# Performance work log

Hardware: AMD Instinct MI355X
Metric: run time of the kernel (lower is better)

The kernel has to match this reference:

```python
import jax, jax.numpy as jnp
import numpy as np

BN_EPS = 1e-5


def setup_inputs() -> dict:
    key = jax.random.key(0)
    ks = jax.random.split(key, 10)
    B, C, L = 16, 512, 1024
    scale = 1.0 / np.sqrt(C)
    inp = {
        "x": jax.random.normal(ks[0], (B, C, L), dtype=jnp.float32),
        "gamma": jnp.ones((C,), jnp.float32),
        "beta": jnp.zeros((C,), jnp.float32),
        "Wq": jax.random.normal(ks[1], (C, C), jnp.float32) * scale,
        "bq": jnp.zeros((C,), jnp.float32),
        "Wk": jax.random.normal(ks[2], (C, C), jnp.float32) * scale,
        "bk": jnp.zeros((C,), jnp.float32),
        "Wv": jax.random.normal(ks[3], (C, C), jnp.float32) * scale,
        "bv": jnp.zeros((C,), jnp.float32),
        "Wp": jax.random.normal(ks[4], (C, C), jnp.float32) * scale,
        "bp": jnp.zeros((C,), jnp.float32),
    }
    return inp


def _pointwise(W, b, h):
    # Conv1d with kernel_size=1 == per-position linear: [C_out,C_in] x [B,C_in,L]
    return jnp.einsum("oc,bcl->bol", W, h) + b[None, :, None]


def reference(x, gamma, beta, Wq, bq, Wk, bk, Wv, bv, Wp, bp):
    B, C, L = x.shape
    # BatchNorm1d (training-mode batch statistics over batch & length dims)
    mean = jnp.mean(x, axis=(0, 2), keepdims=True)
    var = jnp.var(x, axis=(0, 2), keepdims=True)
    hn = (x - mean) * jax.lax.rsqrt(var + BN_EPS)
    hn = hn * gamma[None, :, None] + beta[None, :, None]

    q = _pointwise(Wq, bq, hn)  # [B,C,L]
    k = _pointwise(Wk, bk, hn)
    v = _pointwise(Wv, bv, hn)

    # attn[b,i,j] = sum_c q[b,c,i] k[b,c,j] / sqrt(C); i=query pos, j=key pos
    attn = jnp.einsum("bci,bcj->bij", q, k) * (C ** -0.5)
    attn = jax.nn.softmax(attn, axis=-1)

    # out[b,c,i] = sum_j attn[b,i,j] v[b,c,j]
    h_ = jnp.einsum("bij,bcj->bci", attn, v)
    h_ = _pointwise(Wp, bp, h_)
    return x + h_
```

## Files before the change

### kernel.cpp

```cpp
#include <hip/hip_runtime.h>
#include <hip/hip_bf16.h>


#define BB 16
#define CC 512
#define LL 1024

typedef __bf16 bf16x8 __attribute__((ext_vector_type(8)));
typedef float  f32x4  __attribute__((ext_vector_type(4)));

__device__ inline unsigned short bf16_bits(float f) {
  __hip_bfloat16 h = __float2bfloat16(f);
  return __builtin_bit_cast(unsigned short, h);
}
__device__ inline float bits_lo(unsigned int u) {
  return __builtin_bit_cast(float, u << 16);
}
__device__ inline float bits_hi(unsigned int u) {
  return __builtin_bit_cast(float, u & 0xffff0000u);
}

__global__ __launch_bounds__(256) void bn_stats(
    const float* __restrict__ x, const float* __restrict__ gamma,
    const float* __restrict__ beta, float* __restrict__ scl,
    float* __restrict__ sft) {
  int c = blockIdx.x;
  int t = threadIdx.x;
  float s = 0.f, s2 = 0.f;
  for (int b = 0; b < BB; ++b) {
    float4 v = ((const float4*)(x + ((size_t)(b * CC + c)) * LL))[t];
    s  += v.x + v.y + v.z + v.w;
    s2 += v.x * v.x + v.y * v.y + v.z * v.z + v.w * v.w;
  }
  for (int m = 32; m; m >>= 1) { s += __shfl_xor(s, m, 64); s2 += __shfl_xor(s2, m, 64); }
  __shared__ float rs[4], rs2[4];
  int wave = t >> 6, lane = t & 63;
  if (lane == 0) { rs[wave] = s; rs2[wave] = s2; }
  __syncthreads();
  if (t == 0) {
    float S  = rs[0] + rs[1] + rs[2] + rs[3];
    float S2 = rs2[0] + rs2[1] + rs2[2] + rs2[3];
    float mean = S * (1.f / 16384.f);
    float var  = S2 * (1.f / 16384.f) - mean * mean;
    float sc = gamma[c] * rsqrtf(var + 1e-5f);
    scl[c] = sc;
    sft[c] = beta[c] - mean * sc;
  }
}

__global__ __launch_bounds__(256) void cast4(
    const float* __restrict__ Wq, const float* __restrict__ Wk,
    const float* __restrict__ Wv, const float* __restrict__ Wp,
    __hip_bfloat16* __restrict__ Wqkv, __hip_bfloat16* __restrict__ Wpb) {
  int m = blockIdx.y;
  const float* src = m == 0 ? Wq : m == 1 ? Wk : m == 2 ? Wv : Wp;
  __hip_bfloat16* dst = m < 3 ? Wqkv + (size_t)m * 262144 : Wpb;
  int i = blockIdx.x * 256 + threadIdx.x;
  float4 v = ((const float4*)src)[i];
  ushort4 o;
  o.x = bf16_bits(v.x); o.y = bf16_bits(v.y);
  o.z = bf16_bits(v.z); o.w = bf16_bits(v.w);
  ((ushort4*)dst)[i] = o;
}

__global__ __launch_bounds__(256) void norm_t(
    const float* __restrict__ x, const float* __restrict__ scl,
    const float* __restrict__ sft, __hip_bfloat16* __restrict__ hnT) {
  __shared__ float tile[32][33];
  int l0 = blockIdx.x * 32, c0 = blockIdx.y * 32, b = blockIdx.z;
  int t = threadIdx.x;
#pragma unroll
  for (int i = 0; i < 4; ++i) {
    int idx = t + i * 256;
    int cc = idx >> 5, ll = idx & 31;
    tile[cc][ll] = x[((size_t)(b * CC + c0 + cc)) * LL + l0 + ll];
  }
  __syncthreads();
#pragma unroll
  for (int i = 0; i < 2; ++i) {
    int idx = t + i * 256;
    int ll = idx >> 4, cc = (idx & 15) * 2;
    float v0 = tile[cc][ll] * scl[c0 + cc] + sft[c0 + cc];
    float v1 = tile[cc + 1][ll] * scl[c0 + cc + 1] + sft[c0 + cc + 1];
    ushort2 o; o.x = bf16_bits(v0); o.y = bf16_bits(v1);
    *(ushort2*)(hnT + ((size_t)(b * LL + l0 + ll)) * CC + c0 + cc) = o;
  }
}

__global__ __launch_bounds__(256) void softmax_bf16(__hip_bfloat16* __restrict__ S) {
  int wave = threadIdx.x >> 6, lane = threadIdx.x & 63;
  size_t row = (size_t)blockIdx.x * 4 + wave;
  uint4* p = (uint4*)(S + row * 1024);
  uint4 r0 = p[lane * 2], r1 = p[lane * 2 + 1];
  float f[16];
  unsigned int w[8] = {r0.x, r0.y, r0.z, r0.w, r1.x, r1.y, r1.z, r1.w};
#pragma unroll
  for (int i = 0; i < 8; ++i) { f[2 * i] = bits_lo(w[i]); f[2 * i + 1] = bits_hi(w[i]); }
  float mx = f[0];
#pragma unroll
  for (int i = 1; i < 16; ++i) mx = fmaxf(mx, f[i]);
  for (int m = 32; m; m >>= 1) mx = fmaxf(mx, __shfl_xor(mx, m, 64));
  float s = 0.f;
#pragma unroll
  for (int i = 0; i < 16; ++i) { f[i] = __expf(f[i] - mx); s += f[i]; }
  for (int m = 32; m; m >>= 1) s += __shfl_xor(s, m, 64);
  float inv = 1.f / s;
  unsigned int ow[8];
#pragma unroll
  for (int i = 0; i < 8; ++i) {
    unsigned int lo = bf16_bits(f[2 * i] * inv);
    unsigned int hi = bf16_bits(f[2 * i + 1] * inv);
    ow[i] = lo | (hi << 16);
  }
  uint4 o0 = {ow[0], ow[1], ow[2], ow[3]}, o1 = {ow[4], ow[5], ow[6], ow[7]};
  p[lane * 2] = o0; p[lane * 2 + 1] = o1;
}

__device__ __forceinline__ void gemm_core(
    const __hip_bfloat16* __restrict__ A, int lda,
    const __hip_bfloat16* __restrict__ B, int ldb, int K,
    __hip_bfloat16* sA, __hip_bfloat16* sB, f32x4 (&acc)[4][4]) {
  const int tid = threadIdx.x;
  const int wave = tid >> 6, lane = tid & 63;
  const int wm = (wave >> 1) * 64, wn = (wave & 1) * 64;
  const int row0 = tid >> 2;
  const int ke0 = (((tid & 3) ^ ((tid >> 3) & 3)) * 8);
  const int fr = lane & 15;
  const int q = lane >> 4;
  const int colA = ((q ^ ((fr >> 1) & 3)) * 8);
  for (int k0 = 0; k0 < K; k0 += 32) {
    __syncthreads();
#pragma unroll
    for (int it = 0; it < 2; ++it) {
      const __hip_bfloat16* ga = A + (size_t)(it * 64 + row0) * lda + (k0 + ke0);
      const __hip_bfloat16* gb = B + (size_t)(it * 64 + row0) * ldb + (k0 + ke0);
      __builtin_amdgcn_global_load_lds(
          (__attribute__((address_space(1))) void*)(void*)ga,
          (__attribute__((address_space(3))) void*)(sA + (it * 256 + wave * 64) * 8),
          16, 0, 0);
      __builtin_amdgcn_global_load_lds(
          (__attribute__((address_space(1))) void*)(void*)gb,
          (__attribute__((address_space(3))) void*)(sB + (it * 256 + wave * 64) * 8),
          16, 0, 0);
    }
    __syncthreads();
    bf16x8 af[4], bfr[4];
#pragma unroll
    for (int i = 0; i < 4; ++i) {
      af[i]  = *(const bf16x8*)(sA + (wm + i * 16 + fr) * 32 + colA);
      bfr[i] = *(const bf16x8*)(sB + (wn + i * 16 + fr) * 32 + colA);
    }
#pragma unroll
    for (int i = 0; i < 4; ++i)
#pragma unroll
      for (int j = 0; j < 4; ++j)
        acc[i][j] = __builtin_amdgcn_mfma_f32_16x16x32_bf16(af[i], bfr[j], acc[i][j], 0, 0, 0);
  }
}

__global__ __launch_bounds__(256, 3) void gemm_qkv(
    const __hip_bfloat16* __restrict__ Wb, const __hip_bfloat16* __restrict__ hnT,
    __hip_bfloat16* __restrict__ qT, __hip_bfloat16* __restrict__ kT,
    __hip_bfloat16* __restrict__ vN,
    const float* __restrict__ bq, const float* __restrict__ bk,
    const float* __restrict__ bv) {
  __shared__ __align__(16) __hip_bfloat16 sA[128 * 32];
  __shared__ __align__(16) __hip_bfloat16 sB[128 * 32];
  const int bat = blockIdx.z;
  const int m0 = blockIdx.y * 128, n0 = blockIdx.x * 128;
  f32x4 acc[4][4] = {};
  gemm_core(Wb + (size_t)m0 * 512, 512,
            hnT + (size_t)bat * LL * CC + (size_t)n0 * 512, 512, 512, sA, sB, acc);
  const int lane = threadIdx.x & 63, wave = threadIdx.x >> 6;
  const int wm = (wave >> 1) * 64, wn = (wave & 1) * 64;
  const int crow = (lane >> 4) * 4, ccol = lane & 15;
  const int id = m0 >> 9;
  const int mloc0 = m0 & 511;
  const float* bias = id == 0 ? bq : id == 1 ? bk : bv;
  if (id < 2) {
    __hip_bfloat16* D = (id == 0 ? qT : kT) + (size_t)bat * LL * CC;
#pragma unroll
    for (int i = 0; i < 4; ++i) {
      int mg = mloc0 + wm + i * 16 + crow;
      float bv4[4];
#pragma unroll
      for (int r = 0; r < 4; ++r) bv4[r] = bias[mg + r];
#pragma unroll
      for (int j = 0; j < 4; ++j) {
        int ng = n0 + wn + j * 16 + ccol;
        ushort4 o;
        o.x = bf16_bits(acc[i][j][0] + bv4[0]);
        o.y = bf16_bits(acc[i][j][1] + bv4[1]);
        o.z = bf16_bits(acc[i][j][2] + bv4[2]);
        o.w = bf16_bits(acc[i][j][3] + bv4[3]);
        *(ushort4*)(D + (size_t)ng * 512 + mg) = o;
      }
    }
  } else {
    __hip_bfloat16* D = vN + (size_t)bat * CC * LL;
#pragma unroll
    for (int i = 0; i < 4; ++i) {
      int mg = mloc0 + wm + i * 16 + crow;
      float bv4[4];
#pragma unroll
      for (int r = 0; r < 4; ++r) bv4[r] = bias[mg + r];
#pragma unroll
      for (int j = 0; j < 4; ++j) {
        int ng = n0 + wn + j * 16 + ccol;
#pragma unroll
        for (int r = 0; r < 4; ++r)
          D[(size_t)(mg + r) * 1024 + ng] = __float2bfloat16(acc[i][j][r] + bv4[r]);
      }
    }
  }
}

template <int MODE, bool BIAS>
__global__ __launch_bounds__(256, 3) void gemm_tn(
    const __hip_bfloat16* __restrict__ A, int lda, size_t strideA,
    const __hip_bfloat16* __restrict__ B, int ldb, size_t strideB,
    void* __restrict__ Dp, int ldd, size_t strideD,
    const float* __restrict__ bias, float scale,
    const float* __restrict__ resid, size_t strideR, int K) {
  __shared__ __align__(16) __hip_bfloat16 sA[128 * 32];
  __shared__ __align__(16) __hip_bfloat16 sB[128 * 32];
  const int bat = blockIdx.z;
  const int m0 = blockIdx.y * 128, n0 = blockIdx.x * 128;
  f32x4 acc[4][4] = {};
  gemm_core(A + (size_t)bat * strideA + (size_t)m0 * lda, lda,
            B + (size_t)bat * strideB + (size_t)n0 * ldb, ldb, K, sA, sB, acc);
  const int lane = threadIdx.x & 63, wave = threadIdx.x >> 6;
  const int wm = (wave >> 1) * 64, wn = (wave & 1) * 64;
  const int crow = (lane >> 4) * 4, ccol = lane & 15;
  if constexpr (MODE == 0) {
    __hip_bfloat16* D = (__hip_bfloat16*)Dp + (size_t)bat * strideD;
#pragma unroll
    for (int i = 0; i < 4; ++i) {
      int mg = m0 + wm + i * 16 + crow;
      float bv4[4];
#pragma unroll
      for (int r = 0; r < 4; ++r) bv4[r] = BIAS ? bias[mg + r] : 0.f;
#pragma unroll
      for (int j = 0; j < 4; ++j) {
        int ng = n0 + wn + j * 16 + ccol;
#pragma unroll
        for (int r = 0; r < 4; ++r)
          D[(size_t)(mg + r) * ldd + ng] =
              __float2bfloat16(acc[i][j][r] * scale + bv4[r]);
      }
    }
  } else {
    float* D = (float*)Dp + (size_t)bat * strideD;
#pragma unroll
    for (int i = 0; i < 4; ++i) {
      int mg = m0 + wm + i * 16 + crow;
      float bv4[4];
#pragma unroll
      for (int r = 0; r < 4; ++r) bv4[r] = BIAS ? bias[mg + r] : 0.f;
#pragma unroll
      for (int j = 0; j < 4; ++j) {
        int ng = n0 + wn + j * 16 + ccol;
        const float* rsrc = resid + (size_t)bat * strideR + (size_t)mg * ldd + ng;
        float* dst = D + (size_t)mg * ldd + ng;
#pragma unroll
        for (int r = 0; r < 4; ++r)
          dst[(size_t)r * ldd] = acc[i][j][r] * scale + bv4[r] + rsrc[(size_t)r * ldd];
      }
    }
  }
}

extern "C" void kernel_launch(void* const* d_in, const int* in_sizes, int n_in,
                              void* d_out, int out_size, void* d_ws, size_t ws_size,
                              hipStream_t stream) {
  const float* x     = (const float*)d_in[0];
  const float* gamma = (const float*)d_in[1];
  const float* beta  = (const float*)d_in[2];
  const float* Wq    = (const float*)d_in[3];
  const float* bq    = (const float*)d_in[4];
  const float* Wk    = (const float*)d_in[5];
  const float* bk    = (const float*)d_in[6];
  const float* Wv    = (const float*)d_in[7];
  const float* bv    = (const float*)d_in[8];
  const float* Wp    = (const float*)d_in[9];
  const float* bp    = (const float*)d_in[10];
  float* out = (float*)d_out;

  char* ws = (char*)d_ws;
  float* scl = (float*)ws;
  float* sft = scl + 512;
  __hip_bfloat16* Wqkvb = (__hip_bfloat16*)(ws + 4096);
  __hip_bfloat16* Wpb = Wqkvb + 786432;
  __hip_bfloat16* hnT = Wpb + 262144;
  __hip_bfloat16* qT  = hnT + 8388608;
  __hip_bfloat16* kT  = qT + 8388608;
  __hip_bfloat16* vN  = kT + 8388608;
  __hip_bfloat16* Sb  = vN + 8388608;
  __hip_bfloat16* HT  = hnT;

  bn_stats<<<512, 256, 0, stream>>>(x, gamma, beta, scl, sft);
  cast4<<<dim3(256, 4), 256, 0, stream>>>(Wq, Wk, Wv, Wp, Wqkvb, Wpb);
  norm_t<<<dim3(32, 16, 16), 256, 0, stream>>>(x, scl, sft, hnT);

  const size_t sLC = (size_t)LL * CC;
  const size_t sCL = (size_t)CC * LL;
  const size_t sLLb = (size_t)LL * LL;

  gemm_qkv<<<dim3(8, 12, 16), 256, 0, stream>>>(Wqkvb, hnT, qT, kT, vN, bq, bk, bv);
  gemm_tn<0, false><<<dim3(8, 8, 16), 256, 0, stream>>>(
      qT, 512, sLC, kT, 512, sLC, Sb, 1024, sLLb, nullptr,
      0.04419417382415922f, nullptr, 0, 512);
  softmax_bf16<<<4096, 256, 0, stream>>>(Sb);
  gemm_tn<0, false><<<dim3(4, 8, 16), 256, 0, stream>>>(
      Sb, 1024, sLLb, vN, 1024, sCL, HT, 512, sLC, nullptr, 1.f, nullptr, 0, 1024);
  gemm_tn<3, true><<<dim3(8, 4, 16), 256, 0, stream>>>(
      Wpb, 512, 0, HT, 512, sLC, out, 1024, sCL, bp, 1.f, x, sCL, 512);
}
```

Baseline: 244.2 us.

## Use 256x256-tile triple-buffered GEMM core for QKV and score GEMMs

Adds a 512-thread GEMM core with 256x256 output tiles, three-stage LDS buffering via direct global-to-LDS loads, and explicit waitcnt/barrier scheduling with raised priority around the MFMA block. The QKV projection is relaunched as one flattened GEMM over batch times length, and QK^T uses the new core. The aim is more data reuse per tile and overlap of loads with compute, so the GEMMs spend less time waiting on memory. In exchange it uses more registers and LDS and launches fewer blocks, which may reduce occupancy and leave some CUs idle.

After: 249.5 us. 1.02x slower.

```diff
diff --git a/kernel.cpp b/kernel.cpp
--- a/kernel.cpp
+++ b/kernel.cpp
@@ -158,59 +158,171 @@
   }
 }
 
-__global__ __launch_bounds__(256, 3) void gemm_qkv(
+__device__ __forceinline__ void gemm_core256(
+    const __hip_bfloat16* __restrict__ A, int lda,
+    const __hip_bfloat16* __restrict__ B, int ldb, int K,
+    __hip_bfloat16* sA, __hip_bfloat16* sB, f32x4 (&acc)[8][4]) {
+  const int tid = threadIdx.x;
+  const int wave = tid >> 6, lane = tid & 63;
+  const int row0 = tid >> 2;
+  const int ke0 = (((tid & 3) ^ ((tid >> 3) & 3)) * 8);
+  const int fr = lane & 15;
+  const int q = lane >> 4;
+  const int colA = ((q ^ ((fr >> 1) & 3)) * 8);
+  const int wm = (wave >> 2) * 128, wn = (wave & 3) * 64;
+  const int NT = K >> 5;
+
+  const __hip_bfloat16* ga0 = A + (size_t)row0 * lda + ke0;
+  const __hip_bfloat16* gb0 = B + (size_t)row0 * ldb + ke0;
+  __hip_bfloat16* dA = sA + wave * 512;
+  __hip_bfloat16* dB = sB + wave * 512;
+
+#define STAGE256(tt, ss)                                                       \
+  {                                                                            \
+    const __hip_bfloat16* ga = ga0 + (tt) * 32;                                \
+    const __hip_bfloat16* gb = gb0 + (tt) * 32;                                \
+    __builtin_amdgcn_global_load_lds(                                          \
+        (__attribute__((address_space(1))) void*)(void*)ga,                    \
+        (__attribute__((address_space(3))) void*)(dA + (ss) * 8192), 16, 0, 0);\
+    __builtin_amdgcn_global_load_lds(                                          \
+        (__attribute__((address_space(1))) void*)(void*)(ga + (size_t)128 * lda), \
+        (__attribute__((address_space(3))) void*)(dA + (ss) * 8192 + 4096), 16, 0, 0); \
+    __builtin_amdgcn_global_load_lds(                                          \
+        (__attribute__((address_space(1))) void*)(void*)gb,                    \
+        (__attribute__((address_space(3))) void*)(dB + (ss) * 8192), 16, 0, 0);\
+    __builtin_amdgcn_global_load_lds(                                          \
+        (__attribute__((address_space(1))) void*)(void*)(gb + (size_t)128 * ldb), \
+        (__attribute__((address_space(3))) void*)(dB + (ss) * 8192 + 4096), 16, 0, 0); \
+  }
+
+  STAGE256(0, 0);
+  if (NT > 1) STAGE256(1, 1);
+  if (NT > 2) STAGE256(2, 2);
+
+  int s = 0;
+  for (int t = 0; t < NT; ++t) {
+    if (t < NT - 2) {
+      asm volatile("s_waitcnt vmcnt(8)" ::: "memory");
+    } else if (t == NT - 2) {
+      asm volatile("s_waitcnt vmcnt(4)" ::: "memory");
+    } else {
+      asm volatile("s_waitcnt vmcnt(0)" ::: "memory");
+    }
+    __builtin_amdgcn_s_barrier();
+    __builtin_amdgcn_sched_barrier(0);
+
+    const __hip_bfloat16* pA = sA + s * 8192;
+    const __hip_bfloat16* pB = sB + s * 8192;
+    bf16x8 af[8], bfr[4];
+#pragma unroll
+    for (int i = 0; i < 8; ++i)
+      af[i] = *(const bf16x8*)(pA + (wm + i * 16 + fr) * 32 + colA);
+#pragma unroll
+    for (int j = 0; j < 4; ++j)
+      bfr[j] = *(const bf16x8*)(pB + (wn + j * 16 + fr) * 32 + colA);
+    asm volatile("s_waitcnt lgkmcnt(0)" ::: "memory");
+    __builtin_amdgcn_sched_barrier(0);
+    __builtin_amdgcn_s_barrier();
+    __builtin_amdgcn_sched_barrier(0);
+
+    if (t + 3 < NT) STAGE256(t + 3, s);
+
+    __builtin_amdgcn_s_setprio(1);
+#pragma unroll
+    for (int i = 0; i < 8; ++i)
+#pragma unroll
+      for (int j = 0; j < 4; ++j)
+        acc[i][j] = __builtin_amdgcn_mfma_f32_16x16x32_bf16(af[i], bfr[j], acc[i][j], 0, 0, 0);
+    __builtin_amdgcn_s_setprio(0);
+
+    s = (s == 2) ? 0 : s + 1;
+  }
+#undef STAGE256
+}
+
+__global__ __launch_bounds__(512, 2) void gemm_qkv256(
     const __hip_bfloat16* __restrict__ Wb, const __hip_bfloat16* __restrict__ hnT,
     __hip_bfloat16* __restrict__ qT, __hip_bfloat16* __restrict__ kT,
     __hip_bfloat16* __restrict__ vN,
     const float* __restrict__ bq, const float* __restrict__ bk,
     const float* __restrict__ bv) {
-  __shared__ __align__(16) __hip_bfloat16 sA[128 * 32];
-  __shared__ __align__(16) __hip_bfloat16 sB[128 * 32];
-  const int bat = blockIdx.z;
-  const int m0 = blockIdx.y * 128, n0 = blockIdx.x * 128;
-  f32x4 acc[4][4] = {};
-  gemm_core(Wb + (size_t)m0 * 512, 512,
-            hnT + (size_t)bat * LL * CC + (size_t)n0 * 512, 512, 512, sA, sB, acc);
+  __shared__ __align__(16) __hip_bfloat16 sA[3 * 8192];
+  __shared__ __align__(16) __hip_bfloat16 sB[3 * 8192];
+  const int m0 = blockIdx.y * 256, n0 = blockIdx.x * 256;
+  f32x4 acc[8][4] = {};
+  gemm_core256(Wb + (size_t)m0 * 512, 512, hnT + (size_t)n0 * 512, 512, 512,
+               sA, sB, acc);
   const int lane = threadIdx.x & 63, wave = threadIdx.x >> 6;
-  const int wm = (wave >> 1) * 64, wn = (wave & 1) * 64;
+  const int wm = (wave >> 2) * 128, wn = (wave & 3) * 64;
   const int crow = (lane >> 4) * 4, ccol = lane & 15;
   const int id = m0 >> 9;
-  const int mloc0 = m0 & 511;
+  const int mloc0 = (m0 & 511) + wm;
   const float* bias = id == 0 ? bq : id == 1 ? bk : bv;
   if (id < 2) {
-    __hip_bfloat16* D = (id == 0 ? qT : kT) + (size_t)bat * LL * CC;
-#pragma unroll
-    for (int i = 0; i < 4; ++i) {
-      int mg = mloc0 + wm + i * 16 + crow;
+    __hip_bfloat16* D = id == 0 ? qT : kT;
+#pragma unroll
+    for (int i = 0; i < 8; ++i) {
+      int mg = mloc0 + i * 16 + crow;
       float bv4[4];
 #pragma unroll
       for (int r = 0; r < 4; ++r) bv4[r] = bias[mg + r];
 #pragma unroll
       for (int j = 0; j < 4; ++j) {
-        int ng = n0 + wn + j * 16 + ccol;
+        size_t ng = (size_t)(n0 + wn + j * 16 + ccol);
         ushort4 o;
         o.x = bf16_bits(acc[i][j][0] + bv4[0]);
         o.y = bf16_bits(acc[i][j][1] + bv4[1]);
         o.z = bf16_bits(acc[i][j][2] + bv4[2]);
         o.w = bf16_bits(acc[i][j][3] + bv4[3]);
-        *(ushort4*)(D + (size_t)ng * 512 + mg) = o;
+        *(ushort4*)(D + ng * 512 + mg) = o;
       }
     }
   } else {
-    __hip_bfloat16* D = vN + (size_t)bat * CC * LL;
-#pragma unroll
-    for (int i = 0; i < 4; ++i) {
-      int mg = mloc0 + wm + i * 16 + crow;
+#pragma unroll
+    for (int i = 0; i < 8; ++i) {
+      int mg = mloc0 + i * 16 + crow;
       float bv4[4];
 #pragma unroll
       for (int r = 0; r < 4; ++r) bv4[r] = bias[mg + r];
 #pragma unroll
       for (int j = 0; j < 4; ++j) {
-        int ng = n0 + wn + j * 16 + ccol;
+        int ngf = n0 + wn + j * 16 + ccol;
+        int b = ngf >> 10, l = ngf & 1023;
+        __hip_bfloat16* D = vN + ((size_t)b * CC + mg) * LL + l;
 #pragma unroll
         for (int r = 0; r < 4; ++r)
-          D[(size_t)(mg + r) * 1024 + ng] = __float2bfloat16(acc[i][j][r] + bv4[r]);
+          D[(size_t)r * LL] = __float2bfloat16(acc[i][j][r] + bv4[r]);
       }
+    }
+  }
+}
+
+__global__ __launch_bounds__(512, 2) void gemm_s256(
+    const __hip_bfloat16* __restrict__ qT, const __hip_bfloat16* __restrict__ kT,
+    __hip_bfloat16* __restrict__ Sb) {
+  __shared__ __align__(16) __hip_bfloat16 sA[3 * 8192];
+  __shared__ __align__(16) __hip_bfloat16 sB[3 * 8192];
+  const int bat = blockIdx.z;
+  const int m0 = blockIdx.y * 256, n0 = blockIdx.x * 256;
+  const size_t sLC = (size_t)LL * CC;
+  f32x4 acc[8][4] = {};
+  gemm_core256(qT + (size_t)bat * sLC + (size_t)m0 * 512, 512,
+               kT + (size_t)bat * sLC + (size_t)n0 * 512, 512, 512,
+               sA, sB, acc);
+  const int lane = threadIdx.x & 63, wave = threadIdx.x >> 6;
+  const int wm = (wave >> 2) * 128, wn = (wave & 3) * 64;
+  const int crow = (lane >> 4) * 4, ccol = lane & 15;
+  __hip_bfloat16* D = Sb + (size_t)bat * LL * LL;
+  const float scale = 0.04419417382415922f;
+#pragma unroll
+  for (int i = 0; i < 8; ++i) {
+    int mg = m0 + wm + i * 16 + crow;
+#pragma unroll
+    for (int j = 0; j < 4; ++j) {
+      int ng = n0 + wn + j * 16 + ccol;
+#pragma unroll
+      for (int r = 0; r < 4; ++r)
+        D[(size_t)(mg + r) * LL + ng] = __float2bfloat16(acc[i][j][r] * scale);
     }
   }
 }
@@ -306,10 +418,8 @@
   const size_t sCL = (size_t)CC * LL;
   const size_t sLLb = (size_t)LL * LL;
 
-  gemm_qkv<<<dim3(8, 12, 16), 256, 0, stream>>>(Wqkvb, hnT, qT, kT, vN, bq, bk, bv);
-  gemm_tn<0, false><<<dim3(8, 8, 16), 256, 0, stream>>>(
-      qT, 512, sLC, kT, 512, sLC, Sb, 1024, sLLb, nullptr,
-      0.04419417382415922f, nullptr, 0, 512);
+  gemm_qkv256<<<dim3(64, 6), 512, 0, stream>>>(Wqkvb, hnT, qT, kT, vN, bq, bk, bv);
+  gemm_s256<<<dim3(4, 4, 16), 512, 0, stream>>>(qT, kT, Sb);
   softmax_bf16<<<4096, 256, 0, stream>>>(Sb);
   gemm_tn<0, false><<<dim3(4, 8, 16), 256, 0, stream>>>(
       Sb, 1024, sLLb, vN, 1024, sCL, HT, 512, sLC, nullptr, 1.f, nullptr, 0, 1024);
```
